# Kernel tuning notes

Measured on AMD Instinct MI355X. Metric: run time of the kernel, lower is better.

The kernel has to match this reference:

```python
import jax, jax.numpy as jnp
import numpy as np

NEG_SLOPE = 0.2  # PyG GATConv default negative_slope


def gat_layer(x, edge_index, W, att_src, att_dst, bias):
    """GATConv with self-loops, concat heads. x:[N,F_in], W:[F_in,H*C]."""
    N = x.shape[0]
    H, C = att_src.shape
    loop = jnp.arange(N, dtype=edge_index.dtype)
    src = jnp.concatenate([edge_index[0], loop])  # [E+N]
    dst = jnp.concatenate([edge_index[1], loop])
    h = (x @ W).reshape(N, H, C)                  # [N,H,C]
    a_src = jnp.einsum('nhc,hc->nh', h, att_src)  # [N,H]
    a_dst = jnp.einsum('nhc,hc->nh', h, att_dst)
    e = a_src[src] + a_dst[dst]                   # [E+N,H]
    e = jnp.where(e > 0, e, NEG_SLOPE * e)        # leaky_relu
    # numerically-stable segment softmax over incoming edges of each dst node
    m = jax.ops.segment_max(e, dst, num_segments=N)           # [N,H]
    ex = jnp.exp(e - m[dst])
    denom = jax.ops.segment_sum(ex, dst, num_segments=N)      # [N,H]
    alpha = ex / (denom[dst] + 1e-16)                          # [E+N,H]
    out = jax.ops.segment_sum(h[src] * alpha[:, :, None], dst, num_segments=N)
    return out.reshape(N, H * C) + bias


def setup_inputs() -> dict:
    key = jax.random.key(0)
    ks = jax.random.split(key, 16)
    N, E, F_IN, HID, H, NCLS = 50000, 800000, 128, 64, 4, 40
    HC = H * HID
    s = 0.1
    return {
        'x': jax.random.normal(ks[0], (N, F_IN), jnp.float32),
        'edge_index': jax.random.randint(ks[1], (2, E), 0, N, jnp.int32),
        'W1': jax.random.normal(ks[2], (F_IN, HC), jnp.float32) * s,
        'att_src1': jax.random.normal(ks[3], (H, HID), jnp.float32) * s,
        'att_dst1': jax.random.normal(ks[4], (H, HID), jnp.float32) * s,
        'b1': jnp.zeros((HC,), jnp.float32),
        'W2': jax.random.normal(ks[5], (HC, HC), jnp.float32) * s,
        'att_src2': jax.random.normal(ks[6], (H, HID), jnp.float32) * s,
        'att_dst2': jax.random.normal(ks[7], (H, HID), jnp.float32) * s,
        'b2': jnp.zeros((HC,), jnp.float32),
        'fcW1': jax.random.normal(ks[8], (HC, HID), jnp.float32) * s,
        'fcb1': jnp.zeros((HID,), jnp.float32),
        'fcW2': jax.random.normal(ks[9], (HID, NCLS), jnp.float32) * s,
        'fcb2': jnp.zeros((NCLS,), jnp.float32),
    }


def reference(x, edge_index, W1, att_src1, att_dst1, b1,
              W2, att_src2, att_dst2, b2, fcW1, fcb1, fcW2, fcb2):
    h = gat_layer(x, edge_index, W1, att_src1, att_dst1, b1)
    h = jax.nn.elu(h)
    h = gat_layer(h, edge_index, W2, att_src2, att_dst2, b2)
    h = jax.nn.elu(h)
    h = jnp.maximum(h @ fcW1 + fcb1, 0.0)  # ReLU; dropout is identity in eval
    return h @ fcW2 + fcb2                 # [N, num_classes]
```

## Files before the change

kernel.cpp:

```cpp
#include <hip/hip_runtime.h>

typedef __attribute__((ext_vector_type(8))) _Float16 fp16x8;
typedef __attribute__((ext_vector_type(4))) float f32x4;
typedef __attribute__((ext_vector_type(4))) _Float16 h4;
typedef unsigned int u32;

__device__ __forceinline__ float lrelu(float x) { return x > 0.f ? x : 0.2f * x; }
__device__ __forceinline__ float elu(float x) { return x > 0.f ? x : __expf(x) - 1.f; }

__device__ __forceinline__ void gl2lds16(const void* g, void* l) {
    __builtin_amdgcn_global_load_lds((const __attribute__((address_space(1))) u32*)g,
                                     (__attribute__((address_space(3))) u32*)l, 16, 0, 0);
}

__device__ __forceinline__ void t16t_body(const float* __restrict__ W, _Float16* __restrict__ T,
                                          int N, int Nreal, int t) {
    int lane = t & 63, rem = t >> 6;
    int kk = rem & 1; rem >>= 1;
    int ncg = N / 16;
    int cg = rem % ncg, kc = rem / ncg;
    int k = kc * 64 + kk * 32 + (lane >> 4) * 8;
    int n = cg * 16 + (lane & 15);
    fp16x8 o;
#pragma unroll
    for (int j = 0; j < 8; ++j)
        o[j] = (n < Nreal) ? (_Float16)W[(size_t)(k + j) * Nreal + n] : (_Float16)0.f;
    *(fp16x8*)(T + (size_t)t * 8) = o;
}

__global__ __launch_bounds__(256) void k_prep(const float* __restrict__ W1, _Float16* __restrict__ W1T,
                                              const float* __restrict__ W2, _Float16* __restrict__ W2T,
                                              const float* __restrict__ fcW1, _Float16* __restrict__ fWT,
                                              const float* __restrict__ fcW2, _Float16* __restrict__ f2T,
                                              const int* __restrict__ dst, int* __restrict__ cnt) {
    int b = blockIdx.x, tid = threadIdx.x;
    if (b < 16)      t16t_body(W1, W1T, 256, 256, b * 256 + tid);
    else if (b < 48) t16t_body(W2, W2T, 256, 256, (b - 16) * 256 + tid);
    else if (b < 56) t16t_body(fcW1, fWT, 64, 64, (b - 48) * 256 + tid);
    else if (b < 58) t16t_body(fcW2, f2T, 64, 40, (b - 56) * 256 + tid);
    else             atomicAdd(&cnt[dst[(b - 58) * 256 + tid]], 1);
}

__global__ __launch_bounds__(256) void k_scan_a(const int* __restrict__ cnt, int* __restrict__ s,
                                                int* __restrict__ partial, int N) {
    __shared__ int sh[256];
    int t = threadIdx.x, gid = blockIdx.x * 256 + t;
    sh[t] = gid < N ? cnt[gid] : 0;
    __syncthreads();
    for (int off = 1; off < 256; off <<= 1) {
        int add = (t >= off) ? sh[t - off] : 0;
        __syncthreads();
        sh[t] += add;
        __syncthreads();
    }
    if (gid < N) s[gid] = sh[t];
    if (t == 255) partial[blockIdx.x] = sh[255];
}
__global__ __launch_bounds__(256) void k_scan_bc(const int* __restrict__ s, const int* __restrict__ partial,
                                                 const int* __restrict__ cnt, int* __restrict__ row_ptr,
                                                 int* __restrict__ cursor, int* __restrict__ bcur, int N) {
    __shared__ int red[256];
    int t = threadIdx.x, bid = blockIdx.x;
    int a = 0;
    for (int i = t; i < bid; i += 256) a += partial[i];
    red[t] = a;
    __syncthreads();
    for (int off = 128; off; off >>= 1) {
        if (t < off) red[t] += red[t + off];
        __syncthreads();
    }
    int base = red[0];
    int gid = bid * 256 + t;
    if (gid >= N) return;
    int val = s[gid] + base;
    row_ptr[gid + 1] = val;
    int excl = val - cnt[gid];
    cursor[gid] = excl;
    if ((gid & 511) == 0) bcur[gid >> 9] = excl;
    if (gid == 0) row_ptr[0] = 0;
}

__global__ __launch_bounds__(256) void k_bin(const int* __restrict__ src, const int* __restrict__ dst,
                                             int* __restrict__ bcur, int2* __restrict__ pairbuf, int E) {
    __shared__ int cnt[128], gbase[128], excl[128], cur2[128], sh[128];
    __shared__ int saddr[1024];
    __shared__ int2 spair[1024];
    const int tid = threadIdx.x;
    const int eb = blockIdx.x * 1024;
    if (tid < 128) { cnt[tid] = 0; cur2[tid] = 0; }
    __syncthreads();
    int s_[4], d_[4];
#pragma unroll
    for (int j = 0; j < 4; ++j) {
        int e = eb + j * 256 + tid;
        if (e < E) {
            s_[j] = src[e]; d_[j] = dst[e];
            atomicAdd(&cnt[d_[j] >> 9], 1);
        } else d_[j] = -1;
    }
    __syncthreads();
    if (tid < 128) sh[tid] = cnt[tid];
    __syncthreads();
    for (int off = 1; off < 128; off <<= 1) {
        int add = 0;
        if (tid < 128 && tid >= off) add = sh[tid - off];
        __syncthreads();
        if (tid < 128) sh[tid] += add;
        __syncthreads();
    }
    if (tid < 128) {
        excl[tid] = sh[tid] - cnt[tid];
        if (cnt[tid] > 0) gbase[tid] = atomicAdd(&bcur[tid], cnt[tid]);
    }
    __syncthreads();
#pragma unroll
    for (int j = 0; j < 4; ++j) {
        if (d_[j] >= 0) {
            int b = d_[j] >> 9;
            int r = atomicAdd(&cur2[b], 1);
            int slot = excl[b] + r;
            spair[slot] = make_int2(s_[j], d_[j]);
            saddr[slot] = gbase[b] + r;
        }
    }
    __syncthreads();
    int tot = min(1024, E - eb);
#pragma unroll
    for (int j = 0; j < 4; ++j) {
        int slot = j * 256 + tid;
        if (slot < tot) pairbuf[saddr[slot]] = spair[slot];
    }
}

template<int KV, int NW, int ATT, int AFP32>
__device__ __forceinline__ void gemm_body(int bid,
              const _Float16* __restrict__ Ah, const float* __restrict__ Af,
              const _Float16* __restrict__ BT, _Float16* __restrict__ Chi,
              const float* __restrict__ att_s, const float* __restrict__ att_d,
              float* __restrict__ a_src, float* __restrict__ a_dst,
              int M, int Nc) {
    constexpr int NCG = NW / 16;
    constexpr int CHUNK = NW * 64;
    constexpr int FPW = (CHUNK / 512) / 4;
    __shared__ _Float16 Bs[CHUNK];
    const int m0 = bid * 64;
    const int tid = threadIdx.x;
    const int lane = tid & 63, wv = tid >> 6;
    const int r16 = lane & 15, quad = lane >> 4;
    const int arow = min(m0 + wv * 16 + r16, M - 1);

    f32x4 acc[NCG];
#pragma unroll
    for (int cg = 0; cg < NCG; ++cg) acc[cg] = (f32x4){0, 0, 0, 0};

    constexpr int NCH = KV / 64;
#pragma unroll
    for (int kc = 0; kc < NCH; ++kc) {
        if (kc) __syncthreads();
#pragma unroll
        for (int f = 0; f < FPW; ++f) {
            int fr = wv * FPW + f;
            gl2lds16(BT + (size_t)kc * CHUNK + fr * 512 + lane * 8, &Bs[fr * 512]);
        }
        fp16x8 ar[2];
        if (AFP32) {
            const float* Ap = Af + (size_t)arow * KV + kc * 64 + quad * 8;
#pragma unroll
            for (int kk = 0; kk < 2; ++kk) {
                float4 u0 = *(const float4*)(Ap + kk * 32);
                float4 u1 = *(const float4*)(Ap + kk * 32 + 4);
                fp16x8 h8;
                h8[0] = (_Float16)u0.x; h8[1] = (_Float16)u0.y;
                h8[2] = (_Float16)u0.z; h8[3] = (_Float16)u0.w;
                h8[4] = (_Float16)u1.x; h8[5] = (_Float16)u1.y;
                h8[6] = (_Float16)u1.z; h8[7] = (_Float16)u1.w;
                ar[kk] = h8;
            }
        } else {
            const _Float16* Ahp = Ah + (size_t)arow * KV + kc * 64 + quad * 8;
#pragma unroll
            for (int kk = 0; kk < 2; ++kk) ar[kk] = *(const fp16x8*)(Ahp + kk * 32);
        }
        __syncthreads();
#pragma unroll
        for (int kk = 0; kk < 2; ++kk) {
#pragma unroll
            for (int cg = 0; cg < NCG; ++cg) {
                fp16x8 bh = *(const fp16x8*)(&Bs[(cg * 2 + kk) * 512 + lane * 8]);
                acc[cg] = __builtin_amdgcn_mfma_f32_16x16x32_f16(ar[kk], bh, acc[cg], 0, 0, 0);
            }
        }
    }

    const int rbase = m0 + wv * 16 + quad * 4;

    if (ATT) {
#pragma unroll
        for (int hq = 0; hq < 4; ++hq) {
            float as[4], ad[4];
#pragma unroll
            for (int cg = 0; cg < 4; ++cg) {
                as[cg] = att_s[hq * 64 + cg * 16 + r16];
                ad[cg] = att_d[hq * 64 + cg * 16 + r16];
            }
#pragma unroll
            for (int i = 0; i < 4; ++i) {
                float ps = acc[hq * 4 + 0][i] * as[0] + acc[hq * 4 + 1][i] * as[1]
                         + acc[hq * 4 + 2][i] * as[2] + acc[hq * 4 + 3][i] * as[3];
                float pd = acc[hq * 4 + 0][i] * ad[0] + acc[hq * 4 + 1][i] * ad[1]
                         + acc[hq * 4 + 2][i] * ad[2] + acc[hq * 4 + 3][i] * ad[3];
#pragma unroll
                for (int d = 1; d < 16; d <<= 1) {
                    ps += __shfl_xor(ps, d);
                    pd += __shfl_xor(pd, d);
                }
                int r = rbase + i;
                if (r16 == 0 && r < M) {
                    a_src[(size_t)r * 4 + hq] = ps;
                    a_dst[(size_t)r * 4 + hq] = pd;
                }
            }
        }
    }

#pragma unroll
    for (int cg = 0; cg < NCG; ++cg) {
        int c = cg * 16 + r16;
        if (c >= Nc) continue;
#pragma unroll
        for (int i = 0; i < 4; ++i) {
            int r = rbase + i;
            if (r < M) Chi[(size_t)r * Nc + c] = (_Float16)acc[cg][i];
        }
    }
}

__global__ __launch_bounds__(256, 4)
void k_work1(const float* __restrict__ x, const _Float16* __restrict__ W1T,
             _Float16* __restrict__ h,
             const float* __restrict__ att_s, const float* __restrict__ att_d,
             float* __restrict__ a_src, float* __restrict__ a_dst,
             const int2* __restrict__ pairbuf,
             int* __restrict__ cursor, int* __restrict__ csr,
             int M, int E, int RB) {
    if ((int)blockIdx.x >= RB) {
        int base = (blockIdx.x - RB) * 1024;
#pragma unroll
        for (int j = 0; j < 4; ++j) {
            int i = base + j * 256 + threadIdx.x;
            if (i < E) {
                int2 p = pairbuf[i];
                int pos = atomicAdd(&cursor[p.y], 1);
                csr[pos] = p.x;
            }
        }
        return;
    }
    gemm_body<128, 256, 1, 1>(blockIdx.x, nullptr, x, W1T, h, att_s, att_d, a_src, a_dst, M, 256);
}

__global__ __launch_bounds__(256, 4)
void k_gemm2(const _Float16* __restrict__ Ah, const _Float16* __restrict__ BT,
             _Float16* __restrict__ h,
             const float* __restrict__ att_s, const float* __restrict__ att_d,
             float* __restrict__ a_src, float* __restrict__ a_dst, int M) {
    gemm_body<256, 256, 1, 0>(blockIdx.x, Ah, nullptr, BT, h, att_s, att_d, a_src, a_dst, M, 256);
}

__global__ __launch_bounds__(256, 4)
void k_fc(const _Float16* __restrict__ Ah, const _Float16* __restrict__ BT1,
          const _Float16* __restrict__ BT2, const float* __restrict__ b1,
          const float* __restrict__ b2, float* __restrict__ out, int M) {
    __shared__ _Float16 S[4096 + 64 * 72];
    const int m0 = blockIdx.x * 64;
    const int tid = threadIdx.x;
    const int lane = tid & 63, wv = tid >> 6;
    const int r16 = lane & 15, quad = lane >> 4;
    const int arow = min(m0 + wv * 16 + r16, M - 1);

    f32x4 acc[4];
#pragma unroll
    for (int cg = 0; cg < 4; ++cg) acc[cg] = (f32x4){0, 0, 0, 0};
#pragma unroll
    for (int kc = 0; kc < 4; ++kc) {
        if (kc) __syncthreads();
#pragma unroll
        for (int f = 0; f < 2; ++f) {
            int fr = wv * 2 + f;
            gl2lds16(BT1 + (size_t)kc * 4096 + fr * 512 + lane * 8, &S[fr * 512]);
        }
        fp16x8 ar[2];
        const _Float16* Ahp = Ah + (size_t)arow * 256 + kc * 64 + quad * 8;
#pragma unroll
        for (int kk = 0; kk < 2; ++kk) ar[kk] = *(const fp16x8*)(Ahp + kk * 32);
        __syncthreads();
#pragma unroll
        for (int kk = 0; kk < 2; ++kk) {
#pragma unroll
            for (int cg = 0; cg < 4; ++cg) {
                fp16x8 bh = *(const fp16x8*)(&S[(cg * 2 + kk) * 512 + lane * 8]);
                acc[cg] = __builtin_amdgcn_mfma_f32_16x16x32_f16(ar[kk], bh, acc[cg], 0, 0, 0);
            }
        }
    }
    __syncthreads();
    const int rloc = wv * 16 + quad * 4;
#pragma unroll
    for (int cg = 0; cg < 4; ++cg) {
        int c = cg * 16 + r16;
        float badd = b1[c];
#pragma unroll
        for (int i = 0; i < 4; ++i)
            S[4096 + (rloc + i) * 72 + c] = (_Float16)fmaxf(acc[cg][i] + badd, 0.f);
    }
    __syncthreads();
    const int arow2 = wv * 16 + r16;
    fp16x8 a2[2];
#pragma unroll
    for (int kk = 0; kk < 2; ++kk)
        a2[kk] = *(const fp16x8*)(&S[4096 + arow2 * 72 + kk * 32 + quad * 8]);
    f32x4 acc2[4];
#pragma unroll
    for (int cg = 0; cg < 4; ++cg) acc2[cg] = (f32x4){0, 0, 0, 0};
#pragma unroll
    for (int kk = 0; kk < 2; ++kk) {
#pragma unroll
        for (int cg = 0; cg < 4; ++cg) {
            fp16x8 bh = *(const fp16x8*)(BT2 + (cg * 2 + kk) * 512 + lane * 8);
            acc2[cg] = __builtin_amdgcn_mfma_f32_16x16x32_f16(a2[kk], bh, acc2[cg], 0, 0, 0);
        }
    }
    const int rbase = m0 + wv * 16 + quad * 4;
#pragma unroll
    for (int cg = 0; cg < 4; ++cg) {
        int c = cg * 16 + r16;
        if (c >= 40) continue;
        float badd = b2[c];
#pragma unroll
        for (int i = 0; i < 4; ++i) {
            int r = rbase + i;
            if (r < M) out[(size_t)r * 40 + c] = acc2[cg][i] + badd;
        }
    }
}

__global__ __launch_bounds__(256) void k_aggr8(const _Float16* __restrict__ h, const float* __restrict__ a_src,
                                               const float* __restrict__ a_dst, const int* __restrict__ row_ptr,
                                               const int* __restrict__ csr, const float* __restrict__ bias,
                                               _Float16* __restrict__ o_hi, int N) {
    int n = blockIdx.x * 8 + (threadIdx.x >> 5);
    if (n >= N) return;
    int cl = threadIdx.x & 31;
    int hd = cl >> 3;
    int beg = row_ptr[n], end = row_ptr[n + 1];
    float adh = a_dst[(size_t)4 * n + hd];
    const _Float16* hb = h + (size_t)cl * 8;

    float ws = __expf(lrelu(a_src[(size_t)4 * n + hd] + adh));
    fp16x8 sv = *(const fp16x8*)(hb + (size_t)n * 256);
    float acc[8];
#pragma unroll
    for (int j = 0; j < 8; ++j) acc[j] = ws * (float)sv[j];
    float dn = ws;

    int e = beg;
    for (; e + 4 <= end; e += 4) {
        int s0 = csr[e], s1 = csr[e + 1], s2 = csr[e + 2], s3 = csr[e + 3];
        float z0 = a_src[(size_t)4 * s0 + hd], z1 = a_src[(size_t)4 * s1 + hd];
        float z2 = a_src[(size_t)4 * s2 + hd], z3 = a_src[(size_t)4 * s3 + hd];
        fp16x8 v0 = *(const fp16x8*)(hb + (size_t)s0 * 256);
        fp16x8 v1 = *(const fp16x8*)(hb + (size_t)s1 * 256);
        fp16x8 v2 = *(const fp16x8*)(hb + (size_t)s2 * 256);
        fp16x8 v3 = *(const fp16x8*)(hb + (size_t)s3 * 256);
        float w0 = __expf(lrelu(z0 + adh)), w1 = __expf(lrelu(z1 + adh));
        float w2 = __expf(lrelu(z2 + adh)), w3 = __expf(lrelu(z3 + adh));
        dn += (w0 + w1) + (w2 + w3);
#pragma unroll
        for (int j = 0; j < 8; ++j)
            acc[j] += w0 * (float)v0[j] + w1 * (float)v1[j]
                    + w2 * (float)v2[j] + w3 * (float)v3[j];
    }
    for (; e + 2 <= end; e += 2) {
        int s0 = csr[e], s1 = csr[e + 1];
        float z0 = a_src[(size_t)4 * s0 + hd], z1 = a_src[(size_t)4 * s1 + hd];
        fp16x8 v0 = *(const fp16x8*)(hb + (size_t)s0 * 256);
        fp16x8 v1 = *(const fp16x8*)(hb + (size_t)s1 * 256);
        float w0 = __expf(lrelu(z0 + adh)), w1 = __expf(lrelu(z1 + adh));
        dn += w0 + w1;
#pragma unroll
        for (int j = 0; j < 8; ++j)
            acc[j] += w0 * (float)v0[j] + w1 * (float)v1[j];
    }
    if (e < end) {
        int s0 = csr[e];
        float w0 = __expf(lrelu(a_src[(size_t)4 * s0 + hd] + adh));
        fp16x8 v0 = *(const fp16x8*)(hb + (size_t)s0 * 256);
        dn += w0;
#pragma unroll
        for (int j = 0; j < 8; ++j) acc[j] += w0 * (float)v0[j];
    }

    float inv = 1.f / (dn + 1e-16f);
    float4 b0 = *(const float4*)(bias + cl * 8);
    float4 b1v = *(const float4*)(bias + cl * 8 + 4);
    fp16x8 hi;
    hi[0] = (_Float16)elu(acc[0] * inv + b0.x);
    hi[1] = (_Float16)elu(acc[1] * inv + b0.y);
    hi[2] = (_Float16)elu(acc[2] * inv + b0.z);
    hi[3] = (_Float16)elu(acc[3] * inv + b0.w);
    hi[4] = (_Float16)elu(acc[4] * inv + b1v.x);
    hi[5] = (_Float16)elu(acc[5] * inv + b1v.y);
    hi[6] = (_Float16)elu(acc[6] * inv + b1v.z);
    hi[7] = (_Float16)elu(acc[7] * inv + b1v.w);
    *(fp16x8*)(o_hi + (size_t)n * 256 + cl * 8) = hi;
}

extern "C" void kernel_launch(void* const* d_in, const int* in_sizes, int n_in,
                              void* d_out, int out_size, void* d_ws, size_t ws_size,
                              hipStream_t stream) {
    const int N = 50000, E = 800000, F_IN = 128, HC = 256, HID = 64, NCLS = 40;
    const float* x    = (const float*)d_in[0];
    const int*   ei   = (const int*)d_in[1];
    const float* W1   = (const float*)d_in[2];
    const float* as1  = (const float*)d_in[3];
    const float* ad1  = (const float*)d_in[4];
    const float* b1   = (const float*)d_in[5];
    const float* W2   = (const float*)d_in[6];
    const float* as2  = (const float*)d_in[7];
    const float* ad2  = (const float*)d_in[8];
    const float* b2   = (const float*)d_in[9];
    const float* fcW1 = (const float*)d_in[10];
    const float* fcb1 = (const float*)d_in[11];
    const float* fcW2 = (const float*)d_in[12];
    const float* fcb2 = (const float*)d_in[13];
    float* out = (float*)d_out;

    char* wp = (char*)d_ws;
    auto alloc = [&](size_t b) { char* p = wp; wp += (b + 255) & ~(size_t)255; return p; };
    _Float16* h     = (_Float16*)alloc((size_t)N * HC * 2);
    _Float16* ohi   = (_Float16*)alloc((size_t)N * HC * 2);
    float*  asrc  = (float*)alloc((size_t)N * 4 * 4);
    float*  adst  = (float*)alloc((size_t)N * 4 * 4);
    _Float16* W1T   = (_Float16*)alloc((size_t)F_IN * HC * 2);
    _Float16* W2T   = (_Float16*)alloc((size_t)HC * HC * 2);
    _Float16* fWT   = (_Float16*)alloc((size_t)HC * HID * 2);
    _Float16* f2T   = (_Float16*)alloc((size_t)HID * HID * 2);
    int* cnt     = (int*)alloc((size_t)N * 4);
    int* sbuf    = (int*)alloc((size_t)N * 4);
    int* part    = (int*)alloc(1024);
    int* row_ptr = (int*)alloc(((size_t)N + 1) * 4);
    int* cursor  = (int*)alloc((size_t)N * 4);
    int* csr     = (int*)alloc((size_t)E * 4);
    int* bcur    = (int*)alloc(128 * 4);
    int2* pairs  = (int2*)alloc((size_t)E * 8);

    const int* src = ei;
    const int* dst = ei + E;

    const int rb = (N + 63) / 64;
    const int node_blocks8 = (N + 7) / 8;
    const int bin_blocks = (E + 1023) / 1024;
    const int p2_blocks = (E + 1023) / 1024;

    hipMemsetAsync(cnt, 0, (size_t)N * 4, stream);
    k_prep<<<3183, 256, 0, stream>>>(W1, W1T, W2, W2T, fcW1, fWT, fcW2, f2T, dst, cnt);
    int nb = (N + 255) / 256;
    k_scan_a<<<nb, 256, 0, stream>>>(cnt, sbuf, part, N);
    k_scan_bc<<<nb, 256, 0, stream>>>(sbuf, part, cnt, row_ptr, cursor, bcur, N);
    k_bin<<<bin_blocks, 256, 0, stream>>>(src, dst, bcur, pairs, E);
    k_work1<<<rb + p2_blocks, 256, 0, stream>>>(x, W1T, h, as1, ad1, asrc, adst,
                                                pairs, cursor, csr, N, E, rb);
    k_aggr8<<<node_blocks8, 256, 0, stream>>>(h, asrc, adst, row_ptr, csr, b1, ohi, N);
    k_gemm2<<<rb, 256, 0, stream>>>(ohi, W2T, h, as2, ad2, asrc, adst, N);
    k_aggr8<<<node_blocks8, 256, 0, stream>>>(h, asrc, adst, row_ptr, csr, b2, ohi, N);
    k_fc<<<rb, 256, 0, stream>>>(ohi, fWT, f2T, fcb1, fcb2, out, N);
}
```

Before: 340.0 us.

## Stage full weight matrix in LDS once per 1024-thread block for GEMMs

```diff
diff --git a/kernel.cpp b/kernel.cpp
--- a/kernel.cpp
+++ b/kernel.cpp
@@ -2,7 +2,6 @@
 
 typedef __attribute__((ext_vector_type(8))) _Float16 fp16x8;
 typedef __attribute__((ext_vector_type(4))) float f32x4;
-typedef __attribute__((ext_vector_type(4))) _Float16 h4;
 typedef unsigned int u32;
 
 __device__ __forceinline__ float lrelu(float x) { return x > 0.f ? x : 0.2f * x; }
@@ -132,36 +131,35 @@
     }
 }
 
-template<int KV, int NW, int ATT, int AFP32>
-__device__ __forceinline__ void gemm_body(int bid,
+template<int KV, int ATT, int AFP32>
+__device__ __forceinline__ void pgemm_body(int bid,
               const _Float16* __restrict__ Ah, const float* __restrict__ Af,
               const _Float16* __restrict__ BT, _Float16* __restrict__ Chi,
               const float* __restrict__ att_s, const float* __restrict__ att_d,
               float* __restrict__ a_src, float* __restrict__ a_dst,
-              int M, int Nc) {
-    constexpr int NCG = NW / 16;
-    constexpr int CHUNK = NW * 64;
-    constexpr int FPW = (CHUNK / 512) / 4;
-    __shared__ _Float16 Bs[CHUNK];
-    const int m0 = bid * 64;
+              int M, _Float16* Bs) {
     const int tid = threadIdx.x;
     const int lane = tid & 63, wv = tid >> 6;
+    constexpr int NSEG = KV * 256 * 2 / 1024;
+#pragma unroll
+    for (int i = 0; i < NSEG / 16; ++i) {
+        int seg = i * 16 + wv;
+        gl2lds16(BT + (size_t)seg * 512 + lane * 8, Bs + (size_t)seg * 512);
+    }
+    __syncthreads();
+
+    const int ntiles = (M + 15) >> 4;
+    const int tile = bid * 16 + wv;
+    if (tile >= ntiles) return;
     const int r16 = lane & 15, quad = lane >> 4;
-    const int arow = min(m0 + wv * 16 + r16, M - 1);
-
-    f32x4 acc[NCG];
-#pragma unroll
-    for (int cg = 0; cg < NCG; ++cg) acc[cg] = (f32x4){0, 0, 0, 0};
-
-    constexpr int NCH = KV / 64;
-#pragma unroll
-    for (int kc = 0; kc < NCH; ++kc) {
-        if (kc) __syncthreads();
-#pragma unroll
-        for (int f = 0; f < FPW; ++f) {
-            int fr = wv * FPW + f;
-            gl2lds16(BT + (size_t)kc * CHUNK + fr * 512 + lane * 8, &Bs[fr * 512]);
-        }
+    const int arow = min(tile * 16 + r16, M - 1);
+
+    f32x4 acc[16];
+#pragma unroll
+    for (int cg = 0; cg < 16; ++cg) acc[cg] = (f32x4){0, 0, 0, 0};
+
+#pragma unroll
+    for (int kc = 0; kc < KV / 64; ++kc) {
         fp16x8 ar[2];
         if (AFP32) {
             const float* Ap = Af + (size_t)arow * KV + kc * 64 + quad * 8;
@@ -181,18 +179,17 @@
 #pragma unroll
             for (int kk = 0; kk < 2; ++kk) ar[kk] = *(const fp16x8*)(Ahp + kk * 32);
         }
-        __syncthreads();
 #pragma unroll
         for (int kk = 0; kk < 2; ++kk) {
 #pragma unroll
-            for (int cg = 0; cg < NCG; ++cg) {
-                fp16x8 bh = *(const fp16x8*)(&Bs[(cg * 2 + kk) * 512 + lane * 8]);
+            for (int cg = 0; cg < 16; ++cg) {
+                fp16x8 bh = *(const fp16x8*)(&Bs[((size_t)(kc * 16 + cg) * 2 + kk) * 512 + lane * 8]);
                 acc[cg] = __builtin_amdgcn_mfma_f32_16x16x32_f16(ar[kk], bh, acc[cg], 0, 0, 0);
             }
         }
     }
 
-    const int rbase = m0 + wv * 16 + quad * 4;
+    const int rbase = tile * 16 + quad * 4;
 
     if (ATT) {
 #pragma unroll
@@ -224,30 +221,30 @@
     }
 
 #pragma unroll
-    for (int cg = 0; cg < NCG; ++cg) {
+    for (int cg = 0; cg < 16; ++cg) {
         int c = cg * 16 + r16;
-        if (c >= Nc) continue;
 #pragma unroll
         for (int i = 0; i < 4; ++i) {
             int r = rbase + i;
-            if (r < M) Chi[(size_t)r * Nc + c] = (_Float16)acc[cg][i];
-        }
-    }
-}
-
-__global__ __launch_bounds__(256, 4)
+            if (r < M) Chi[(size_t)r * 256 + c] = (_Float16)acc[cg][i];
+        }
+    }
+}
+
+__global__ __launch_bounds__(1024, 4)
 void k_work1(const float* __restrict__ x, const _Float16* __restrict__ W1T,
              _Float16* __restrict__ h,
              const float* __restrict__ att_s, const float* __restrict__ att_d,
              float* __restrict__ a_src, float* __restrict__ a_dst,
              const int2* __restrict__ pairbuf,
              int* __restrict__ cursor, int* __restrict__ csr,
-             int M, int E, int RB) {
-    if ((int)blockIdx.x >= RB) {
-        int base = (blockIdx.x - RB) * 1024;
+             int M, int E, int FB) {
+    __shared__ _Float16 Bs[128 * 256];
+    if ((int)blockIdx.x < FB) {
+        int base = blockIdx.x * 4096;
 #pragma unroll
         for (int j = 0; j < 4; ++j) {
-            int i = base + j * 256 + threadIdx.x;
+            int i = base + j * 1024 + threadIdx.x;
             if (i < E) {
                 int2 p = pairbuf[i];
                 int pos = atomicAdd(&cursor[p.y], 1);
@@ -256,69 +253,73 @@
         }
         return;
     }
-    gemm_body<128, 256, 1, 1>(blockIdx.x, nullptr, x, W1T, h, att_s, att_d, a_src, a_dst, M, 256);
-}
-
-__global__ __launch_bounds__(256, 4)
+    pgemm_body<128, 1, 1>(blockIdx.x - FB, nullptr, x, W1T, h,
+                          att_s, att_d, a_src, a_dst, M, Bs);
+}
+
+__global__ __launch_bounds__(1024, 4)
 void k_gemm2(const _Float16* __restrict__ Ah, const _Float16* __restrict__ BT,
              _Float16* __restrict__ h,
              const float* __restrict__ att_s, const float* __restrict__ att_d,
              float* __restrict__ a_src, float* __restrict__ a_dst, int M) {
-    gemm_body<256, 256, 1, 0>(blockIdx.x, Ah, nullptr, BT, h, att_s, att_d, a_src, a_dst, M, 256);
-}
-
-__global__ __launch_bounds__(256, 4)
+    __shared__ _Float16 Bs[256 * 256];
+    pgemm_body<256, 1, 0>(blockIdx.x, Ah, nullptr, BT, h,
+                          att_s, att_d, a_src, a_dst, M, Bs);
+}
+
+__global__ __launch_bounds__(1024, 4)
 void k_fc(const _Float16* __restrict__ Ah, const _Float16* __restrict__ BT1,
           const _Float16* __restrict__ BT2, const float* __restrict__ b1,
           const float* __restrict__ b2, float* __restrict__ out, int M) {
-    __shared__ _Float16 S[4096 + 64 * 72];
-    const int m0 = blockIdx.x * 64;
-    const int tid = threadIdx.x;
-    const int lane = tid & 63, wv = tid >> 6;
+    __shared__ _Float16 B1s[256 * 64];
+    __shared__ _Float16 B2s[64 * 64];
+    __shared__ _Float16 Ts[16 * 16 * 72];
+    const int tid = threadIdx.x, lane = tid & 63, wv = tid >> 6;
+#pragma unroll
+    for (int i = 0; i < 2; ++i) {
+        int seg = i * 16 + wv;
+        gl2lds16(BT1 + (size_t)seg * 512 + lane * 8, B1s + (size_t)seg * 512);
+    }
+    if (wv < 8) gl2lds16(BT2 + (size_t)wv * 512 + lane * 8, B2s + (size_t)wv * 512);
+    __syncthreads();
+
+    const int ntiles = (M + 15) >> 4;
+    const int tile = blockIdx.x * 16 + wv;
+    if (tile >= ntiles) return;
     const int r16 = lane & 15, quad = lane >> 4;
-    const int arow = min(m0 + wv * 16 + r16, M - 1);
+    const int arow = min(tile * 16 + r16, M - 1);
 
     f32x4 acc[4];
 #pragma unroll
     for (int cg = 0; cg < 4; ++cg) acc[cg] = (f32x4){0, 0, 0, 0};
 #pragma unroll
     for (int kc = 0; kc < 4; ++kc) {
-        if (kc) __syncthreads();
-#pragma unroll
-        for (int f = 0; f < 2; ++f) {
-            int fr = wv * 2 + f;
-            gl2lds16(BT1 + (size_t)kc * 4096 + fr * 512 + lane * 8, &S[fr * 512]);
-        }
         fp16x8 ar[2];
         const _Float16* Ahp = Ah + (size_t)arow * 256 + kc * 64 + quad * 8;
 #pragma unroll
         for (int kk = 0; kk < 2; ++kk) ar[kk] = *(const fp16x8*)(Ahp + kk * 32);
-        __syncthreads();
 #pragma unroll
         for (int kk = 0; kk < 2; ++kk) {
 #pragma unroll
             for (int cg = 0; cg < 4; ++cg) {
-                fp16x8 bh = *(const fp16x8*)(&S[(cg * 2 + kk) * 512 + lane * 8]);
+                fp16x8 bh = *(const fp16x8*)(&B1s[((size_t)(kc * 4 + cg) * 2 + kk) * 512 + lane * 8]);
                 acc[cg] = __builtin_amdgcn_mfma_f32_16x16x32_f16(ar[kk], bh, acc[cg], 0, 0, 0);
             }
         }
     }
-    __syncthreads();
-    const int rloc = wv * 16 + quad * 4;
+    _Float16* tw = Ts + (size_t)wv * 1152;
 #pragma unroll
     for (int cg = 0; cg < 4; ++cg) {
         int c = cg * 16 + r16;
         float badd = b1[c];
 #pragma unroll
         for (int i = 0; i < 4; ++i)
-            S[4096 + (rloc + i) * 72 + c] = (_Float16)fmaxf(acc[cg][i] + badd, 0.f);
-    }
-    __syncthreads();
-    const int arow2 = wv * 16 + r16;
+            tw[(quad * 4 + i) * 72 + c] = (_Float16)fmaxf(acc[cg][i] + badd, 0.f);
+    }
     fp16x8 a2[2];
 #pragma unroll
     for (int kk = 0; kk < 2; ++kk)
-        a2[kk] = *(const fp16x8*)(&S[4096 + arow2 * 72 + kk * 32 + quad * 8]);
+        a2[kk] = *(const fp16x8*)(&tw[r16 * 72 + kk * 32 + quad * 8]);
     f32x4 acc2[4];
 #pragma unroll
     for (int cg = 0; cg < 4; ++cg) acc2[cg] = (f32x4){0, 0, 0, 0};
@@ -326,11 +327,11 @@
     for (int kk = 0; kk < 2; ++kk) {
 #pragma unroll
         for (int cg = 0; cg < 4; ++cg) {
-            fp16x8 bh = *(const fp16x8*)(BT2 + (cg * 2 + kk) * 512 + lane * 8);
+            fp16x8 bh = *(const fp16x8*)(&B2s[((size_t)cg * 2 + kk) * 512 + lane * 8]);
             acc2[cg] = __builtin_amdgcn_mfma_f32_16x16x32_f16(a2[kk], bh, acc2[cg], 0, 0, 0);
         }
     }
-    const int rbase = m0 + wv * 16 + quad * 4;
+    const int rbase = tile * 16 + quad * 4;
 #pragma unroll
     for (int cg = 0; cg < 4; ++cg) {
         int c = cg * 16 + r16;
@@ -457,10 +458,10 @@
     const int* src = ei;
     const int* dst = ei + E;
 
-    const int rb = (N + 63) / 64;
     const int node_blocks8 = (N + 7) / 8;
     const int bin_blocks = (E + 1023) / 1024;
-    const int p2_blocks = (E + 1023) / 1024;
+    const int fb = (E + 4095) / 4096;
+    const int fc_blocks = ((N + 15) / 16 + 15) / 16;
 
     hipMemsetAsync(cnt, 0, (size_t)N * 4, stream);
     k_prep<<<3183, 256, 0, stream>>>(W1, W1T, W2, W2T, fcW1, fWT, fcW2, f2T, dst, cnt);
@@ -468,10 +469,10 @@
     k_scan_a<<<nb, 256, 0, stream>>>(cnt, sbuf, part, N);
     k_scan_bc<<<nb, 256, 0, stream>>>(sbuf, part, cnt, row_ptr, cursor, bcur, N);
     k_bin<<<bin_blocks, 256, 0, stream>>>(src, dst, bcur, pairs, E);
-    k_work1<<<rb + p2_blocks, 256, 0, stream>>>(x, W1T, h, as1, ad1, asrc, adst,
-                                                pairs, cursor, csr, N, E, rb);
+    k_work1<<<fb + 256, 1024, 0, stream>>>(x, W1T, h, as1, ad1, asrc, adst,
+                                           pairs, cursor, csr, N, E, fb);
     k_aggr8<<<node_blocks8, 256, 0, stream>>>(h, asrc, adst, row_ptr, csr, b1, ohi, N);
-    k_gemm2<<<rb, 256, 0, stream>>>(ohi, W2T, h, as2, ad2, asrc, adst, N);
+    k_gemm2<<<256, 1024, 0, stream>>>(ohi, W2T, h, as2, ad2, asrc, adst, N);
     k_aggr8<<<node_blocks8, 256, 0, stream>>>(h, asrc, adst, row_ptr, csr, b2, ohi, N);
-    k_fc<<<rb, 256, 0, stream>>>(ohi, fWT, f2T, fcb1, fcb2, out, N);
-}
+    k_fc<<<fc_blocks, 1024, 0, stream>>>(ohi, fWT, f2T, fcb1, fcb2, out, N);
+}
```

New measurement: 346.3 us. About the same (+1.8%).

## Slice feature buffers by 32-column blocks and pin each slice to one XCD

Applied to the files above, without the earlier changes.

```diff
diff --git a/kernel.cpp b/kernel.cpp
--- a/kernel.cpp
+++ b/kernel.cpp
@@ -2,7 +2,6 @@
 
 typedef __attribute__((ext_vector_type(8))) _Float16 fp16x8;
 typedef __attribute__((ext_vector_type(4))) float f32x4;
-typedef __attribute__((ext_vector_type(4))) _Float16 h4;
 typedef unsigned int u32;
 
 __device__ __forceinline__ float lrelu(float x) { return x > 0.f ? x : 0.2f * x; }
@@ -138,7 +137,7 @@
               const _Float16* __restrict__ BT, _Float16* __restrict__ Chi,
               const float* __restrict__ att_s, const float* __restrict__ att_d,
               float* __restrict__ a_src, float* __restrict__ a_dst,
-              int M, int Nc) {
+              int M) {
     constexpr int NCG = NW / 16;
     constexpr int CHUNK = NW * 64;
     constexpr int FPW = (CHUNK / 512) / 4;
@@ -177,9 +176,9 @@
                 ar[kk] = h8;
             }
         } else {
-            const _Float16* Ahp = Ah + (size_t)arow * KV + kc * 64 + quad * 8;
-#pragma unroll
-            for (int kk = 0; kk < 2; ++kk) ar[kk] = *(const fp16x8*)(Ahp + kk * 32);
+#pragma unroll
+            for (int kk = 0; kk < 2; ++kk)
+                ar[kk] = *(const fp16x8*)(Ah + ((size_t)(kc * 2 + kk) * M + arow) * 32 + quad * 8);
         }
         __syncthreads();
 #pragma unroll
@@ -225,12 +224,12 @@
 
 #pragma unroll
     for (int cg = 0; cg < NCG; ++cg) {
-        int c = cg * 16 + r16;
-        if (c >= Nc) continue;
+        const int sl = cg >> 1;
+        const int c32 = (cg & 1) * 16 + r16;
 #pragma unroll
         for (int i = 0; i < 4; ++i) {
             int r = rbase + i;
-            if (r < M) Chi[(size_t)r * Nc + c] = (_Float16)acc[cg][i];
+            if (r < M) Chi[((size_t)sl * M + r) * 32 + c32] = (_Float16)acc[cg][i];
         }
     }
 }
@@ -256,7 +255,7 @@
         }
         return;
     }
-    gemm_body<128, 256, 1, 1>(blockIdx.x, nullptr, x, W1T, h, att_s, att_d, a_src, a_dst, M, 256);
+    gemm_body<128, 256, 1, 1>(blockIdx.x, nullptr, x, W1T, h, att_s, att_d, a_src, a_dst, M);
 }
 
 __global__ __launch_bounds__(256, 4)
@@ -264,7 +263,7 @@
              _Float16* __restrict__ h,
              const float* __restrict__ att_s, const float* __restrict__ att_d,
              float* __restrict__ a_src, float* __restrict__ a_dst, int M) {
-    gemm_body<256, 256, 1, 0>(blockIdx.x, Ah, nullptr, BT, h, att_s, att_d, a_src, a_dst, M, 256);
+    gemm_body<256, 256, 1, 0>(blockIdx.x, Ah, nullptr, BT, h, att_s, att_d, a_src, a_dst, M);
 }
 
 __global__ __launch_bounds__(256, 4)
@@ -290,9 +289,9 @@
             gl2lds16(BT1 + (size_t)kc * 4096 + fr * 512 + lane * 8, &S[fr * 512]);
         }
         fp16x8 ar[2];
-        const _Float16* Ahp = Ah + (size_t)arow * 256 + kc * 64 + quad * 8;
-#pragma unroll
-        for (int kk = 0; kk < 2; ++kk) ar[kk] = *(const fp16x8*)(Ahp + kk * 32);
+#pragma unroll
+        for (int kk = 0; kk < 2; ++kk)
+            ar[kk] = *(const fp16x8*)(Ah + ((size_t)(kc * 2 + kk) * M + arow) * 32 + quad * 8);
         __syncthreads();
 #pragma unroll
         for (int kk = 0; kk < 2; ++kk) {
@@ -344,75 +343,80 @@
     }
 }
 
-__global__ __launch_bounds__(256) void k_aggr8(const _Float16* __restrict__ h, const float* __restrict__ a_src,
-                                               const float* __restrict__ a_dst, const int* __restrict__ row_ptr,
-                                               const int* __restrict__ csr, const float* __restrict__ bias,
-                                               _Float16* __restrict__ o_hi, int N) {
-    int n = blockIdx.x * 8 + (threadIdx.x >> 5);
-    if (n >= N) return;
-    int cl = threadIdx.x & 31;
-    int hd = cl >> 3;
-    int beg = row_ptr[n], end = row_ptr[n + 1];
-    float adh = a_dst[(size_t)4 * n + hd];
-    const _Float16* hb = h + (size_t)cl * 8;
-
-    float ws = __expf(lrelu(a_src[(size_t)4 * n + hd] + adh));
-    fp16x8 sv = *(const fp16x8*)(hb + (size_t)n * 256);
-    float acc[8];
-#pragma unroll
-    for (int j = 0; j < 8; ++j) acc[j] = ws * (float)sv[j];
-    float dn = ws;
-
-    int e = beg;
-    for (; e + 4 <= end; e += 4) {
-        int s0 = csr[e], s1 = csr[e + 1], s2 = csr[e + 2], s3 = csr[e + 3];
-        float z0 = a_src[(size_t)4 * s0 + hd], z1 = a_src[(size_t)4 * s1 + hd];
-        float z2 = a_src[(size_t)4 * s2 + hd], z3 = a_src[(size_t)4 * s3 + hd];
-        fp16x8 v0 = *(const fp16x8*)(hb + (size_t)s0 * 256);
-        fp16x8 v1 = *(const fp16x8*)(hb + (size_t)s1 * 256);
-        fp16x8 v2 = *(const fp16x8*)(hb + (size_t)s2 * 256);
-        fp16x8 v3 = *(const fp16x8*)(hb + (size_t)s3 * 256);
-        float w0 = __expf(lrelu(z0 + adh)), w1 = __expf(lrelu(z1 + adh));
-        float w2 = __expf(lrelu(z2 + adh)), w3 = __expf(lrelu(z3 + adh));
-        dn += (w0 + w1) + (w2 + w3);
-#pragma unroll
-        for (int j = 0; j < 8; ++j)
-            acc[j] += w0 * (float)v0[j] + w1 * (float)v1[j]
-                    + w2 * (float)v2[j] + w3 * (float)v3[j];
-    }
-    for (; e + 2 <= end; e += 2) {
-        int s0 = csr[e], s1 = csr[e + 1];
-        float z0 = a_src[(size_t)4 * s0 + hd], z1 = a_src[(size_t)4 * s1 + hd];
-        fp16x8 v0 = *(const fp16x8*)(hb + (size_t)s0 * 256);
-        fp16x8 v1 = *(const fp16x8*)(hb + (size_t)s1 * 256);
-        float w0 = __expf(lrelu(z0 + adh)), w1 = __expf(lrelu(z1 + adh));
-        dn += w0 + w1;
-#pragma unroll
-        for (int j = 0; j < 8; ++j)
-            acc[j] += w0 * (float)v0[j] + w1 * (float)v1[j];
-    }
-    if (e < end) {
-        int s0 = csr[e];
-        float w0 = __expf(lrelu(a_src[(size_t)4 * s0 + hd] + adh));
-        fp16x8 v0 = *(const fp16x8*)(hb + (size_t)s0 * 256);
-        dn += w0;
-#pragma unroll
-        for (int j = 0; j < 8; ++j) acc[j] += w0 * (float)v0[j];
-    }
-
-    float inv = 1.f / (dn + 1e-16f);
-    float4 b0 = *(const float4*)(bias + cl * 8);
-    float4 b1v = *(const float4*)(bias + cl * 8 + 4);
-    fp16x8 hi;
-    hi[0] = (_Float16)elu(acc[0] * inv + b0.x);
-    hi[1] = (_Float16)elu(acc[1] * inv + b0.y);
-    hi[2] = (_Float16)elu(acc[2] * inv + b0.z);
-    hi[3] = (_Float16)elu(acc[3] * inv + b0.w);
-    hi[4] = (_Float16)elu(acc[4] * inv + b1v.x);
-    hi[5] = (_Float16)elu(acc[5] * inv + b1v.y);
-    hi[6] = (_Float16)elu(acc[6] * inv + b1v.z);
-    hi[7] = (_Float16)elu(acc[7] * inv + b1v.w);
-    *(fp16x8*)(o_hi + (size_t)n * 256 + cl * 8) = hi;
+#define ACH 64
+__global__ __launch_bounds__(256) void k_aggr11(const _Float16* __restrict__ h,
+        const float* __restrict__ a_src, const float* __restrict__ a_dst,
+        const int* __restrict__ row_ptr, const int* __restrict__ csr,
+        const float* __restrict__ bias, _Float16* __restrict__ o,
+        int* __restrict__ wcur, int N) {
+    int xcd;
+    asm volatile("s_getreg_b32 %0, hwreg(HW_REG_XCC_ID)" : "=s"(xcd));
+    xcd &= 7;
+    const int tid = threadIdx.x;
+    const int gi = tid >> 2, L = tid & 3;
+    const int hd = xcd >> 1;
+    const int nch = (N + ACH - 1) / ACH;
+    const _Float16* hb = h + (size_t)xcd * N * 32 + L * 8;
+    float bv[8];
+    {
+        float4 b0 = *(const float4*)(bias + xcd * 32 + L * 8);
+        float4 b1v = *(const float4*)(bias + xcd * 32 + L * 8 + 4);
+        bv[0] = b0.x; bv[1] = b0.y; bv[2] = b0.z; bv[3] = b0.w;
+        bv[4] = b1v.x; bv[5] = b1v.y; bv[6] = b1v.z; bv[7] = b1v.w;
+    }
+    __shared__ int chsh;
+    for (;;) {
+        __syncthreads();
+        if (tid == 0) chsh = atomicAdd(&wcur[xcd], 1);
+        __syncthreads();
+        int ch = chsh;
+        if (ch >= nch) return;
+        int n = ch * ACH + gi;
+        if (n >= N) continue;
+        int beg = row_ptr[n], end = row_ptr[n + 1];
+        float ad = a_dst[(size_t)n * 4 + hd];
+        float ws = __expf(lrelu(a_src[(size_t)n * 4 + hd] + ad));
+        fp16x8 sv = *(const fp16x8*)(hb + (size_t)n * 32);
+        float acc[8];
+#pragma unroll
+        for (int j = 0; j < 8; ++j) acc[j] = ws * (float)sv[j];
+        float dn = ws;
+        int e = beg;
+        for (; e + 4 <= end; e += 4) {
+            int s0 = __builtin_nontemporal_load(csr + e);
+            int s1 = __builtin_nontemporal_load(csr + e + 1);
+            int s2 = __builtin_nontemporal_load(csr + e + 2);
+            int s3 = __builtin_nontemporal_load(csr + e + 3);
+            float z0 = a_src[(size_t)s0 * 4 + hd];
+            float z1 = a_src[(size_t)s1 * 4 + hd];
+            float z2 = a_src[(size_t)s2 * 4 + hd];
+            float z3 = a_src[(size_t)s3 * 4 + hd];
+            fp16x8 v0 = *(const fp16x8*)(hb + (size_t)s0 * 32);
+            fp16x8 v1 = *(const fp16x8*)(hb + (size_t)s1 * 32);
+            fp16x8 v2 = *(const fp16x8*)(hb + (size_t)s2 * 32);
+            fp16x8 v3 = *(const fp16x8*)(hb + (size_t)s3 * 32);
+            float w0 = __expf(lrelu(z0 + ad)), w1 = __expf(lrelu(z1 + ad));
+            float w2 = __expf(lrelu(z2 + ad)), w3 = __expf(lrelu(z3 + ad));
+            dn += (w0 + w1) + (w2 + w3);
+#pragma unroll
+            for (int j = 0; j < 8; ++j)
+                acc[j] += w0 * (float)v0[j] + w1 * (float)v1[j]
+                        + w2 * (float)v2[j] + w3 * (float)v3[j];
+        }
+        for (; e < end; ++e) {
+            int s0 = csr[e];
+            float w0 = __expf(lrelu(a_src[(size_t)s0 * 4 + hd] + ad));
+            fp16x8 v0 = *(const fp16x8*)(hb + (size_t)s0 * 32);
+            dn += w0;
+#pragma unroll
+            for (int j = 0; j < 8; ++j) acc[j] += w0 * (float)v0[j];
+        }
+        float inv = 1.f / (dn + 1e-16f);
+        fp16x8 hi;
+#pragma unroll
+        for (int j = 0; j < 8; ++j) hi[j] = (_Float16)elu(acc[j] * inv + bv[j]);
+        __builtin_nontemporal_store(hi, (fp16x8*)(o + ((size_t)xcd * N + n) * 32 + L * 8));
+    }
 }
 
 extern "C" void kernel_launch(void* const* d_in, const int* in_sizes, int n_in,
@@ -453,16 +457,17 @@
     int* csr     = (int*)alloc((size_t)E * 4);
     int* bcur    = (int*)alloc(128 * 4);
     int2* pairs  = (int2*)alloc((size_t)E * 8);
+    int* wcur    = (int*)alloc(64);
 
     const int* src = ei;
     const int* dst = ei + E;
 
     const int rb = (N + 63) / 64;
-    const int node_blocks8 = (N + 7) / 8;
     const int bin_blocks = (E + 1023) / 1024;
     const int p2_blocks = (E + 1023) / 1024;
 
     hipMemsetAsync(cnt, 0, (size_t)N * 4, stream);
+    hipMemsetAsync(wcur, 0, 64, stream);
     k_prep<<<3183, 256, 0, stream>>>(W1, W1T, W2, W2T, fcW1, fWT, fcW2, f2T, dst, cnt);
     int nb = (N + 255) / 256;
     k_scan_a<<<nb, 256, 0, stream>>>(cnt, sbuf, part, N);
@@ -470,8 +475,8 @@
     k_bin<<<bin_blocks, 256, 0, stream>>>(src, dst, bcur, pairs, E);
     k_work1<<<rb + p2_blocks, 256, 0, stream>>>(x, W1T, h, as1, ad1, asrc, adst,
                                                 pairs, cursor, csr, N, E, rb);
-    k_aggr8<<<node_blocks8, 256, 0, stream>>>(h, asrc, adst, row_ptr, csr, b1, ohi, N);
+    k_aggr11<<<2048, 256, 0, stream>>>(h, asrc, adst, row_ptr, csr, b1, ohi, wcur, N);
     k_gemm2<<<rb, 256, 0, stream>>>(ohi, W2T, h, as2, ad2, asrc, adst, N);
-    k_aggr8<<<node_blocks8, 256, 0, stream>>>(h, asrc, adst, row_ptr, csr, b2, ohi, N);
+    k_aggr11<<<2048, 256, 0, stream>>>(h, asrc, adst, row_ptr, csr, b2, ohi, wcur + 8, N);
     k_fc<<<rb, 256, 0, stream>>>(ohi, fWT, f2T, fcb1, fcb2, out, N);
 }
```

Measured after the change: 488.0 us. 1.44x slower.

## Fuse second GAT aggregation with the FC head into one kernel

Applied to the files above, without the earlier changes.

```diff
diff --git a/kernel.cpp b/kernel.cpp
--- a/kernel.cpp
+++ b/kernel.cpp
@@ -2,7 +2,7 @@
 
 typedef __attribute__((ext_vector_type(8))) _Float16 fp16x8;
 typedef __attribute__((ext_vector_type(4))) float f32x4;
-typedef __attribute__((ext_vector_type(4))) _Float16 h4;
+typedef __attribute__((ext_vector_type(2))) _Float16 h2v;
 typedef unsigned int u32;
 
 __device__ __forceinline__ float lrelu(float x) { return x > 0.f ? x : 0.2f * x; }
@@ -11,6 +11,23 @@
 __device__ __forceinline__ void gl2lds16(const void* g, void* l) {
     __builtin_amdgcn_global_load_lds((const __attribute__((address_space(1))) u32*)g,
                                      (__attribute__((address_space(3))) u32*)l, 16, 0, 0);
+}
+
+__device__ __forceinline__ float dot8(const fp16x8& a, const fp16x8& b) {
+#if __has_builtin(__builtin_amdgcn_fdot2)
+    const h2v* ap = (const h2v*)&a;
+    const h2v* bp = (const h2v*)&b;
+    float p = __builtin_amdgcn_fdot2(ap[0], bp[0], 0.f, false);
+    p = __builtin_amdgcn_fdot2(ap[1], bp[1], p, false);
+    p = __builtin_amdgcn_fdot2(ap[2], bp[2], p, false);
+    p = __builtin_amdgcn_fdot2(ap[3], bp[3], p, false);
+    return p;
+#else
+    float p = 0.f;
+#pragma unroll
+    for (int j = 0; j < 8; ++j) p += (float)a[j] * (float)b[j];
+    return p;
+#endif
 }
 
 __device__ __forceinline__ void t16t_body(const float* __restrict__ W, _Float16* __restrict__ T,
@@ -30,15 +47,25 @@
 
 __global__ __launch_bounds__(256) void k_prep(const float* __restrict__ W1, _Float16* __restrict__ W1T,
                                               const float* __restrict__ W2, _Float16* __restrict__ W2T,
-                                              const float* __restrict__ fcW1, _Float16* __restrict__ fWT,
-                                              const float* __restrict__ fcW2, _Float16* __restrict__ f2T,
+                                              const float* __restrict__ fcW1, _Float16* __restrict__ fl1,
+                                              const float* __restrict__ fcW2, _Float16* __restrict__ f2l,
                                               const int* __restrict__ dst, int* __restrict__ cnt) {
     int b = blockIdx.x, tid = threadIdx.x;
     if (b < 16)      t16t_body(W1, W1T, 256, 256, b * 256 + tid);
     else if (b < 48) t16t_body(W2, W2T, 256, 256, (b - 16) * 256 + tid);
-    else if (b < 56) t16t_body(fcW1, fWT, 64, 64, (b - 48) * 256 + tid);
-    else if (b < 58) t16t_body(fcW2, f2T, 64, 40, (b - 56) * 256 + tid);
-    else             atomicAdd(&cnt[dst[(b - 58) * 256 + tid]], 1);
+    else if (b < 56) {
+        int idx = (b - 48) * 256 + tid;
+        int o = idx >> 5, c0 = (idx & 31) * 8;
+        fp16x8 v;
+#pragma unroll
+        for (int j = 0; j < 8; ++j) v[j] = (_Float16)fcW1[(size_t)(c0 + j) * 64 + o];
+        *(fp16x8*)(fl1 + (size_t)o * 256 + c0) = v;
+    } else if (b < 57) {
+        for (int i = tid; i < 2560; i += 256) {
+            int k = i >> 6, o = i & 63;
+            f2l[i] = (_Float16)fcW2[(size_t)o * 40 + k];
+        }
+    } else atomicAdd(&cnt[dst[(b - 57) * 256 + tid]], 1);
 }
 
 __global__ __launch_bounds__(256) void k_scan_a(const int* __restrict__ cnt, int* __restrict__ s,
@@ -267,83 +294,6 @@
     gemm_body<256, 256, 1, 0>(blockIdx.x, Ah, nullptr, BT, h, att_s, att_d, a_src, a_dst, M, 256);
 }
 
-__global__ __launch_bounds__(256, 4)
-void k_fc(const _Float16* __restrict__ Ah, const _Float16* __restrict__ BT1,
-          const _Float16* __restrict__ BT2, const float* __restrict__ b1,
-          const float* __restrict__ b2, float* __restrict__ out, int M) {
-    __shared__ _Float16 S[4096 + 64 * 72];
-    const int m0 = blockIdx.x * 64;
-    const int tid = threadIdx.x;
-    const int lane = tid & 63, wv = tid >> 6;
-    const int r16 = lane & 15, quad = lane >> 4;
-    const int arow = min(m0 + wv * 16 + r16, M - 1);
-
-    f32x4 acc[4];
-#pragma unroll
-    for (int cg = 0; cg < 4; ++cg) acc[cg] = (f32x4){0, 0, 0, 0};
-#pragma unroll
-    for (int kc = 0; kc < 4; ++kc) {
-        if (kc) __syncthreads();
-#pragma unroll
-        for (int f = 0; f < 2; ++f) {
-            int fr = wv * 2 + f;
-            gl2lds16(BT1 + (size_t)kc * 4096 + fr * 512 + lane * 8, &S[fr * 512]);
-        }
-        fp16x8 ar[2];
-        const _Float16* Ahp = Ah + (size_t)arow * 256 + kc * 64 + quad * 8;
-#pragma unroll
-        for (int kk = 0; kk < 2; ++kk) ar[kk] = *(const fp16x8*)(Ahp + kk * 32);
-        __syncthreads();
-#pragma unroll
-        for (int kk = 0; kk < 2; ++kk) {
-#pragma unroll
-            for (int cg = 0; cg < 4; ++cg) {
-                fp16x8 bh = *(const fp16x8*)(&S[(cg * 2 + kk) * 512 + lane * 8]);
-                acc[cg] = __builtin_amdgcn_mfma_f32_16x16x32_f16(ar[kk], bh, acc[cg], 0, 0, 0);
-            }
-        }
-    }
-    __syncthreads();
-    const int rloc = wv * 16 + quad * 4;
-#pragma unroll
-    for (int cg = 0; cg < 4; ++cg) {
-        int c = cg * 16 + r16;
-        float badd = b1[c];
-#pragma unroll
-        for (int i = 0; i < 4; ++i)
-            S[4096 + (rloc + i) * 72 + c] = (_Float16)fmaxf(acc[cg][i] + badd, 0.f);
-    }
-    __syncthreads();
-    const int arow2 = wv * 16 + r16;
-    fp16x8 a2[2];
-#pragma unroll
-    for (int kk = 0; kk < 2; ++kk)
-        a2[kk] = *(const fp16x8*)(&S[4096 + arow2 * 72 + kk * 32 + quad * 8]);
-    f32x4 acc2[4];
-#pragma unroll
-    for (int cg = 0; cg < 4; ++cg) acc2[cg] = (f32x4){0, 0, 0, 0};
-#pragma unroll
-    for (int kk = 0; kk < 2; ++kk) {
-#pragma unroll
-        for (int cg = 0; cg < 4; ++cg) {
-            fp16x8 bh = *(const fp16x8*)(BT2 + (cg * 2 + kk) * 512 + lane * 8);
-            acc2[cg] = __builtin_amdgcn_mfma_f32_16x16x32_f16(a2[kk], bh, acc2[cg], 0, 0, 0);
-        }
-    }
-    const int rbase = m0 + wv * 16 + quad * 4;
-#pragma unroll
-    for (int cg = 0; cg < 4; ++cg) {
-        int c = cg * 16 + r16;
-        if (c >= 40) continue;
-        float badd = b2[c];
-#pragma unroll
-        for (int i = 0; i < 4; ++i) {
-            int r = rbase + i;
-            if (r < M) out[(size_t)r * 40 + c] = acc2[cg][i] + badd;
-        }
-    }
-}
-
 __global__ __launch_bounds__(256) void k_aggr8(const _Float16* __restrict__ h, const float* __restrict__ a_src,
                                                const float* __restrict__ a_dst, const int* __restrict__ row_ptr,
                                                const int* __restrict__ csr, const float* __restrict__ bias,
@@ -413,6 +363,112 @@
     hi[6] = (_Float16)elu(acc[6] * inv + b1v.z);
     hi[7] = (_Float16)elu(acc[7] * inv + b1v.w);
     *(fp16x8*)(o_hi + (size_t)n * 256 + cl * 8) = hi;
+}
+
+__global__ __launch_bounds__(512, 8) void k_aggr_fc(const _Float16* __restrict__ h,
+        const float* __restrict__ a_src, const float* __restrict__ a_dst,
+        const int* __restrict__ row_ptr, const int* __restrict__ csr,
+        const float* __restrict__ bias,
+        const _Float16* __restrict__ fl1g, const _Float16* __restrict__ f2lg,
+        const float* __restrict__ fcb1, const float* __restrict__ fcb2,
+        float* __restrict__ out, int N) {
+    __shared__ _Float16 fl1[64 * 256];
+    __shared__ _Float16 f2l[40 * 64];
+    const int tid = threadIdx.x, lane = tid & 63, wv = tid >> 6;
+#pragma unroll
+    for (int i = 0; i < 4; ++i)
+        gl2lds16(fl1g + (size_t)(i * 8 + wv) * 512 + lane * 8, fl1 + (size_t)(i * 8 + wv) * 512);
+    if (wv < 5) gl2lds16(f2lg + (size_t)wv * 512 + lane * 8, f2l + (size_t)wv * 512);
+    __syncthreads();
+
+    int n = blockIdx.x * 16 + (tid >> 5);
+    if (n >= N) return;
+    int cl = tid & 31;
+    int hd = cl >> 3;
+    int beg = row_ptr[n], end = row_ptr[n + 1];
+    float adh = a_dst[(size_t)4 * n + hd];
+    const _Float16* hb = h + (size_t)cl * 8;
+
+    float ws = __expf(lrelu(a_src[(size_t)4 * n + hd] + adh));
+    fp16x8 sv = *(const fp16x8*)(hb + (size_t)n * 256);
+    float acc[8];
+#pragma unroll
+    for (int j = 0; j < 8; ++j) acc[j] = ws * (float)sv[j];
+    float dn = ws;
+
+    int e = beg;
+    for (; e + 4 <= end; e += 4) {
+        int s0 = csr[e], s1 = csr[e + 1], s2 = csr[e + 2], s3 = csr[e + 3];
+        float z0 = a_src[(size_t)4 * s0 + hd], z1 = a_src[(size_t)4 * s1 + hd];
+        float z2 = a_src[(size_t)4 * s2 + hd], z3 = a_src[(size_t)4 * s3 + hd];
+        fp16x8 v0 = *(const fp16x8*)(hb + (size_t)s0 * 256);
+        fp16x8 v1 = *(const fp16x8*)(hb + (size_t)s1 * 256);
+        fp16x8 v2 = *(const fp16x8*)(hb + (size_t)s2 * 256);
+        fp16x8 v3 = *(const fp16x8*)(hb + (size_t)s3 * 256);
+        float w0 = __expf(lrelu(z0 + adh)), w1 = __expf(lrelu(z1 + adh));
+        float w2 = __expf(lrelu(z2 + adh)), w3 = __expf(lrelu(z3 + adh));
+        dn += (w0 + w1) + (w2 + w3);
+#pragma unroll
+        for (int j = 0; j < 8; ++j)
+            acc[j] += w0 * (float)v0[j] + w1 * (float)v1[j]
+                    + w2 * (float)v2[j] + w3 * (float)v3[j];
+    }
+    for (; e + 2 <= end; e += 2) {
+        int s0 = csr[e], s1 = csr[e + 1];
+        float z0 = a_src[(size_t)4 * s0 + hd], z1 = a_src[(size_t)4 * s1 + hd];
+        fp16x8 v0 = *(const fp16x8*)(hb + (size_t)s0 * 256);
+        fp16x8 v1 = *(const fp16x8*)(hb + (size_t)s1 * 256);
+        float w0 = __expf(lrelu(z0 + adh)), w1 = __expf(lrelu(z1 + adh));
+        dn += w0 + w1;
+#pragma unroll
+        for (int j = 0; j < 8; ++j)
+            acc[j] += w0 * (float)v0[j] + w1 * (float)v1[j];
+    }
+    if (e < end) {
+        int s0 = csr[e];
+        float w0 = __expf(lrelu(a_src[(size_t)4 * s0 + hd] + adh));
+        fp16x8 v0 = *(const fp16x8*)(hb + (size_t)s0 * 256);
+        dn += w0;
+#pragma unroll
+        for (int j = 0; j < 8; ++j) acc[j] += w0 * (float)v0[j];
+    }
+
+    float inv = 1.f / (dn + 1e-16f);
+    float4 b0 = *(const float4*)(bias + cl * 8);
+    float4 b1v = *(const float4*)(bias + cl * 8 + 4);
+    float r[8];
+    r[0] = elu(acc[0] * inv + b0.x);  r[1] = elu(acc[1] * inv + b0.y);
+    r[2] = elu(acc[2] * inv + b0.z);  r[3] = elu(acc[3] * inv + b0.w);
+    r[4] = elu(acc[4] * inv + b1v.x); r[5] = elu(acc[5] * inv + b1v.y);
+    r[6] = elu(acc[6] * inv + b1v.z); r[7] = elu(acc[7] * inv + b1v.w);
+    fp16x8 rh;
+#pragma unroll
+    for (int j = 0; j < 8; ++j) rh[j] = (_Float16)r[j];
+
+    float t0 = 0.f, t1 = 0.f;
+#pragma unroll
+    for (int o = 0; o < 64; ++o) {
+        fp16x8 w8 = *(const fp16x8*)(fl1 + o * 256 + cl * 8);
+        float p = dot8(rh, w8);
+        p += __shfl_xor(p, 1);  p += __shfl_xor(p, 2);  p += __shfl_xor(p, 4);
+        p += __shfl_xor(p, 8);  p += __shfl_xor(p, 16);
+        float tv = fmaxf(p + fcb1[o], 0.f);
+        if ((o >> 1) == cl) { if (o & 1) t1 = tv; else t0 = tv; }
+    }
+    float o0 = 0.f, o1 = 0.f;
+#pragma unroll
+    for (int k = 0; k < 40; ++k) {
+        float w0 = (float)f2l[k * 64 + cl * 2];
+        float w1 = (float)f2l[k * 64 + cl * 2 + 1];
+        float p = t0 * w0 + t1 * w1;
+        p += __shfl_xor(p, 1);  p += __shfl_xor(p, 2);  p += __shfl_xor(p, 4);
+        p += __shfl_xor(p, 8);  p += __shfl_xor(p, 16);
+        float v = p + fcb2[k];
+        if (k == cl) o0 = v;
+        if (k == cl + 32) o1 = v;
+    }
+    out[(size_t)n * 40 + cl] = o0;
+    if (cl < 8) out[(size_t)n * 40 + 32 + cl] = o1;
 }
 
 extern "C" void kernel_launch(void* const* d_in, const int* in_sizes, int n_in,
@@ -443,8 +499,8 @@
     float*  adst  = (float*)alloc((size_t)N * 4 * 4);
     _Float16* W1T   = (_Float16*)alloc((size_t)F_IN * HC * 2);
     _Float16* W2T   = (_Float16*)alloc((size_t)HC * HC * 2);
-    _Float16* fWT   = (_Float16*)alloc((size_t)HC * HID * 2);
-    _Float16* f2T   = (_Float16*)alloc((size_t)HID * HID * 2);
+    _Float16* fl1g  = (_Float16*)alloc((size_t)HID * HC * 2);
+    _Float16* f2lg  = (_Float16*)alloc((size_t)NCLS * HID * 2);
     int* cnt     = (int*)alloc((size_t)N * 4);
     int* sbuf    = (int*)alloc((size_t)N * 4);
     int* part    = (int*)alloc(1024);
@@ -459,11 +515,12 @@
 
     const int rb = (N + 63) / 64;
     const int node_blocks8 = (N + 7) / 8;
+    const int aggrfc_blocks = (N + 15) / 16;
     const int bin_blocks = (E + 1023) / 1024;
     const int p2_blocks = (E + 1023) / 1024;
 
     hipMemsetAsync(cnt, 0, (size_t)N * 4, stream);
-    k_prep<<<3183, 256, 0, stream>>>(W1, W1T, W2, W2T, fcW1, fWT, fcW2, f2T, dst, cnt);
+    k_prep<<<3182, 256, 0, stream>>>(W1, W1T, W2, W2T, fcW1, fl1g, fcW2, f2lg, dst, cnt);
     int nb = (N + 255) / 256;
     k_scan_a<<<nb, 256, 0, stream>>>(cnt, sbuf, part, N);
     k_scan_bc<<<nb, 256, 0, stream>>>(sbuf, part, cnt, row_ptr, cursor, bcur, N);
@@ -472,6 +529,6 @@
                                                 pairs, cursor, csr, N, E, rb);
     k_aggr8<<<node_blocks8, 256, 0, stream>>>(h, asrc, adst, row_ptr, csr, b1, ohi, N);
     k_gemm2<<<rb, 256, 0, stream>>>(ohi, W2T, h, as2, ad2, asrc, adst, N);
-    k_aggr8<<<node_blocks8, 256, 0, stream>>>(h, asrc, adst, row_ptr, csr, b2, ohi, N);
-    k_fc<<<rb, 256, 0, stream>>>(ohi, fWT, f2T, fcb1, fcb2, out, N);
-}
+    k_aggr_fc<<<aggrfc_blocks, 512, 0, stream>>>(h, asrc, adst, row_ptr, csr, b2,
+                                                 fl1g, f2lg, fcb1, fcb2, out, N);
+}
```

Result: slower. 443.2 us (+30.4%).
